# Kernel tuning notes

Hardware: AMD Instinct MI355X
Metric: run time of the kernel (lower is better)

The kernel has to match this reference:

```python
import jax, jax.numpy as jnp
import numpy as np

E = 1024  # hidden_size
H = 16    # num_heads
D = E // H  # head_dim
LN_EPS = 1e-5


def setup_inputs() -> dict:
    key = jax.random.key(0)
    ks = jax.random.split(key, 7)
    B, S = 4, 2048
    scale = 1.0 / np.sqrt(E)
    return {
        "txt_emb": jax.random.normal(ks[0], (B, S, E), dtype=jnp.float32),
        "in_proj_w": jax.random.normal(ks[1], (3 * E, E), dtype=jnp.float32) * scale,
        "in_proj_b": jnp.zeros((3 * E,), dtype=jnp.float32),
        "out_proj_w": jax.random.normal(ks[2], (E, E), dtype=jnp.float32) * scale,
        "out_proj_b": jnp.zeros((E,), dtype=jnp.float32),
        "ln_gamma": jnp.ones((E,), dtype=jnp.float32),
        "ln_beta": jnp.zeros((E,), dtype=jnp.float32),
    }


def _layer_norm(x, gamma, beta):
    mu = jnp.mean(x, axis=-1, keepdims=True)
    var = jnp.var(x, axis=-1, keepdims=True)
    return (x - mu) * jax.lax.rsqrt(var + LN_EPS) * gamma + beta


def reference(txt_emb, in_proj_w, in_proj_b, out_proj_w, out_proj_b, ln_gamma, ln_beta):
    B, S, _ = txt_emb.shape
    # joint QKV projection (torch nn.MultiheadAttention semantics: x @ W.T + b)
    qkv = jnp.einsum('bse,fe->bsf', txt_emb, in_proj_w) + in_proj_b  # [B,S,3E]
    q, k, v = jnp.split(qkv, 3, axis=-1)
    # [B,H,S,D]
    q = q.reshape(B, S, H, D).transpose(0, 2, 1, 3)
    k = k.reshape(B, S, H, D).transpose(0, 2, 1, 3)
    v = v.reshape(B, S, H, D).transpose(0, 2, 1, 3)
    scores = jnp.einsum('bhqd,bhkd->bhqk', q, k) / np.sqrt(D)  # [B,H,S,S]
    causal = jnp.tril(jnp.ones((S, S), dtype=bool))
    scores = jnp.where(causal, scores, jnp.float32(-jnp.inf))
    attn = jax.nn.softmax(scores, axis=-1)
    ctx = jnp.einsum('bhqk,bhkd->bhqd', attn, v)  # [B,H,S,D]
    ctx = ctx.transpose(0, 2, 1, 3).reshape(B, S, E)
    attn_out = jnp.einsum('bse,fe->bsf', ctx, out_proj_w) + out_proj_b
    return _layer_norm(txt_emb + attn_out, ln_gamma, ln_beta)
```

## Files before the change

### kernel.cpp

```cpp
#include <hip/hip_runtime.h>
#include <hip/hip_bf16.h>
#include <stdint.h>

#define B_   4
#define S_   2048
#define E_   1024
#define H_   16
#define D_   64
#define M_   (B_ * S_)
#define E3_  (3 * E_)

#define QSCALE 0.18033688011112042f

typedef __bf16 bf16_t;
typedef bf16_t bf16x8 __attribute__((ext_vector_type(8)));
typedef float  f32x4  __attribute__((ext_vector_type(4)));
typedef float  f32x16 __attribute__((ext_vector_type(16)));

__device__ __forceinline__ ushort f2bf(float f) {
  union { float f; uint32_t u; } v; v.f = f;
  uint32_t r = v.u + 0x7fffu + ((v.u >> 16) & 1u);
  return (ushort)(r >> 16);
}

__device__ __forceinline__ float bf2f(ushort u) {
  union { uint32_t u; float f; } v; v.u = ((uint32_t)u) << 16;
  return v.f;
}

__device__ __forceinline__ unsigned cvtpk(float lo, float hi_) {
  unsigned d;
  asm("v_cvt_pk_bf16_f32 %0, %1, %2" : "=v"(d) : "v"(lo), "v"(hi_));
  return d;
}

__device__ __forceinline__ void gload_lds16(const void* g, void* l) {
  __builtin_amdgcn_global_load_lds((const __attribute__((address_space(1))) void*)g,
                                   (__attribute__((address_space(3))) void*)l,
                                   16, 0, 0);
}

__global__ __launch_bounds__(256) void cvt_all(const float* __restrict__ x,
                                               const float* __restrict__ w_in,
                                               const float* __restrict__ w_out,
                                               ushort* __restrict__ xb,
                                               ushort* __restrict__ winb,
                                               ushort* __restrict__ woutb) {
  const int stride = gridDim.x * blockDim.x;
  for (int i = blockIdx.x * blockDim.x + threadIdx.x; i < 3145728; i += stride) {
    const float* src; ushort* dst; int j; float sc = 1.f;
    if (i < 2097152)      { src = x;     dst = xb;    j = i; }
    else if (i < 2883584) { src = w_in;  dst = winb;  j = i - 2097152; if (j < 262144) sc = QSCALE; }
    else                  { src = w_out; dst = woutb; j = i - 2883584; }
    float4 v = reinterpret_cast<const float4*>(src)[j];
    ushort4 o;
    o.x = f2bf(v.x * sc); o.y = f2bf(v.y * sc); o.z = f2bf(v.z * sc); o.w = f2bf(v.w * sc);
    reinterpret_cast<ushort4*>(dst)[j] = o;
  }
}

template <int MODE>
__global__ __launch_bounds__(256) void gemm_bt2(const ushort* __restrict__ A,
                                                const ushort* __restrict__ Bt,
                                                const float* __restrict__ bias,
                                                void* __restrict__ out0,
                                                ushort* __restrict__ vTout,
                                                int Ndim, int K) {
  __shared__ __align__(16) char lds[3][16384];

  const int tid  = threadIdx.x;
  const int lane = tid & 63, wid = tid >> 6;
  const int w = wid;
  const int wr = wid >> 1, wc = wid & 1;

  const int nx  = Ndim >> 7;
  const int nwg = gridDim.x;
  const int b0  = blockIdx.x;
  const int nb  = (b0 & 7) * (nwg >> 3) + (b0 >> 3);
  const int bm  = (nb / nx) * 128, bn = (nb % nx) * 128;

  const int srow  = tid >> 2;
  const int sslot = (tid & 3) ^ (srow & 3) ^ ((srow >> 2) & 3);
  const ushort* aS = A  + (size_t)(bm + srow) * K + sslot * 8;
  const ushort* bS = Bt + (size_t)(bn + srow) * K + sslot * 8;

#define STAGE_A(T, BUF)                                                          \
  do {                                                                           \
    gload_lds16(aS + (size_t)(T) * 32,              (void*)((BUF) + w * 1024));  \
    gload_lds16(aS + (size_t)(T) * 32 + 64 * K,     (void*)((BUF) + 4096 + w * 1024)); \
  } while (0)
#define STAGE_B(T, BUF)                                                          \
  do {                                                                           \
    gload_lds16(bS + (size_t)(T) * 32,              (void*)((BUF) + 8192 + w * 1024)); \
    gload_lds16(bS + (size_t)(T) * 32 + 64 * K,     (void*)((BUF) + 12288 + w * 1024)); \
  } while (0)

  const int lr15 = lane & 15;
  const int ksub = lane >> 4;
  const int slot = (ksub ^ (lr15 & 3) ^ ((lr15 >> 2) & 3)) * 16;
  const int arow_b = (wr * 64 + lr15) * 64;
  const int brow_b = 8192 + (wc * 64 + lr15) * 64;

#define LDA4(BUF)                                                                \
  do {                                                                           \
    _Pragma("unroll")                                                            \
    for (int rb = 0; rb < 4; ++rb)                                               \
      af[rb] = *(const bf16x8*)((BUF) + arow_b + rb * 1024 + slot);              \
  } while (0)
#define LDB2(BUF, CB)                                                            \
  do {                                                                           \
    _Pragma("unroll")                                                            \
    for (int n = 0; n < 2; ++n)                                                  \
      bfr[n] = *(const bf16x8*)((BUF) + brow_b + ((CB) + n) * 1024 + slot);      \
  } while (0)
#define MFMA8(CB)                                                                \
  do {                                                                           \
    __builtin_amdgcn_s_setprio(1);                                               \
    _Pragma("unroll")                                                            \
    for (int rb = 0; rb < 4; ++rb)                                               \
      _Pragma("unroll")                                                          \
      for (int n = 0; n < 2; ++n)                                                \
        acc[rb][(CB) + n] = __builtin_amdgcn_mfma_f32_16x16x32_bf16(             \
            af[rb], bfr[n], acc[rb][(CB) + n], 0, 0, 0);                         \
    __builtin_amdgcn_s_setprio(0);                                               \
  } while (0)

  f32x4 acc[4][4] = {};
  bf16x8 af[4], bfr[2];

  char* buf0 = &lds[0][0];
  char* buf1 = &lds[1][0];
  char* buf2 = &lds[2][0];

  const int nt = K >> 5;

  STAGE_A(0, buf0); STAGE_B(0, buf0);
  STAGE_A(1, buf1); STAGE_B(1, buf1);
  asm volatile("s_waitcnt vmcnt(4)" ::: "memory");
  __builtin_amdgcn_s_barrier();
  __builtin_amdgcn_sched_barrier(0);

  for (int t = 0; t < nt; ++t) {
    if (t < nt - 2) STAGE_A(t + 2, buf2);
    LDA4(buf0);
    LDB2(buf0, 0);
    __builtin_amdgcn_s_barrier();
    asm volatile("s_waitcnt lgkmcnt(0)" ::: "memory");
    __builtin_amdgcn_sched_barrier(0);
    MFMA8(0);
    __builtin_amdgcn_s_barrier();
    __builtin_amdgcn_sched_barrier(0);
    if (t < nt - 2) STAGE_B(t + 2, buf2);
    LDB2(buf0, 2);
    __builtin_amdgcn_s_barrier();
    asm volatile("s_waitcnt lgkmcnt(0)" ::: "memory");
    __builtin_amdgcn_sched_barrier(0);
    MFMA8(2);
    if (t < nt - 2) asm volatile("s_waitcnt vmcnt(4)" ::: "memory");
    else if (t == nt - 2) asm volatile("s_waitcnt vmcnt(0)" ::: "memory");
    __builtin_amdgcn_s_barrier();
    __builtin_amdgcn_sched_barrier(0);
    char* tmp = buf0; buf0 = buf1; buf1 = buf2; buf2 = tmp;
  }

#pragma unroll
  for (int rb = 0; rb < 4; ++rb) {
#pragma unroll
    for (int cb = 0; cb < 4; ++cb) {
      const int col = bn + wc * 64 + cb * 16 + lr15;
      float bv = bias[col];
      if (MODE == 1 && col < 1024) bv *= QSCALE;
      const int row0 = bm + wr * 64 + rb * 16 + ksub * 4;
      if (MODE == 0) {
#pragma unroll
        for (int r = 0; r < 4; ++r)
          ((ushort*)out0)[(size_t)(row0 + r) * Ndim + col] = f2bf(acc[rb][cb][r] + bv);
      } else {
        if (col < 2048) {
#pragma unroll
          for (int r = 0; r < 4; ++r)
            ((ushort*)out0)[(size_t)(row0 + r) * 2048 + col] = f2bf(acc[rb][cb][r] + bv);
        } else {
          ushort4 vv;
          vv.x = f2bf(acc[rb][cb][0] + bv);
          vv.y = f2bf(acc[rb][cb][1] + bv);
          vv.z = f2bf(acc[rb][cb][2] + bv);
          vv.w = f2bf(acc[rb][cb][3] + bv);
          const size_t vidx = ((size_t)((row0 >> 11) * 1024 + (col - 2048))) * 2048 + (row0 & 2047);
          *reinterpret_cast<ushort4*>(&vTout[vidx]) = vv;
        }
      }
    }
  }
#undef STAGE_A
#undef STAGE_B
#undef LDA4
#undef LDB2
#undef MFMA8
}

__global__ __launch_bounds__(512) void attn_causal(const ushort* __restrict__ qk,
                                                   const ushort* __restrict__ vT,
                                                   ushort* __restrict__ ctx) {
  __shared__ __align__(16) char lds[2][32768];

  const int tid = threadIdx.x;
  const int w = tid >> 6, lane = tid & 63;
  const int l31 = lane & 31, hi = lane >> 5;

  const int bid = blockIdx.x;
  const int bh = (bid & 7) * 8 + ((bid >> 3) & 7);
  const int g6 = bid >> 6;
  const int qb = (g6 < 4) ? (7 - g6) : (g6 - 4);
  const int b = bh >> 4, h = bh & 15;
  const int qw = qb * 256 + w * 32;
  const int q_g = qw + l31;
  const int my_tmax = (qw + 31) >> 6;
  const int U = 2 * qb + 2;

  const ushort* qrow = qk + (size_t)(b * S_ + q_g) * 2048 + h * 64;
  bf16x8 qf[4];
#pragma unroll
  for (int st = 0; st < 4; ++st)
    qf[st] = *reinterpret_cast<const bf16x8*>(qrow + st * 16 + hi * 8);

  const int srow = tid >> 3;
  const int swz  = ((tid & 7) * 16) ^ ((srow & 7) << 4);
  const char* kbase = (const char*)qk + ((size_t)(b * S_ + srow) * 2048 + 1024 + h * 64) * 2 + swz;
  const char* vbase = (const char*)vT + ((size_t)(bh * 64 + srow) * 2048) * 2 + swz;

  f32x16 Ot0 = {}, Ot1 = {};
  float m_r = -__builtin_inff(), l_r = 0.f;

  const int kswz = ((l31 & 7) << 4);

#define STAGE_PAIR(U2, BUFI)                                                            \
  do {                                                                                  \
    const size_t t0_ = (size_t)(U2) * 2;                                                \
    gload_lds16(kbase + t0_ * 262144,          &lds[BUFI][w * 1024]);                   \
    gload_lds16(kbase + (t0_ + 1) * 262144,    &lds[BUFI][8192 + w * 1024]);            \
    gload_lds16(vbase + t0_ * 128,             &lds[BUFI][16384 + w * 1024]);           \
    gload_lds16(vbase + t0_ * 128 + 128,       &lds[BUFI][24576 + w * 1024]);           \
  } while (0)

  STAGE_PAIR(0, 0);
  for (int u = 0; u < U; ++u) {
    const int bufi = u & 1;
    if (u < U - 1) {
      STAGE_PAIR(u + 1, bufi ^ 1);
      asm volatile("s_waitcnt vmcnt(4)" ::: "memory");
    } else {
      asm volatile("s_waitcnt vmcnt(0)" ::: "memory");
    }
    __builtin_amdgcn_s_barrier();
    __builtin_amdgcn_sched_barrier(0);

#pragma unroll
    for (int s = 0; s < 2; ++s) {
      const int t = 2 * u + s;
      if (t <= my_tmax) {
        const char* Kt = &lds[bufi][s * 8192];
        const char* Vp = &lds[bufi][16384 + s * 8192];

        f32x16 T0 = {}, T1 = {};
#pragma unroll
        for (int st = 0; st < 4; ++st) {
          const int cb = (st * 32 + hi * 16) ^ kswz;
          bf16x8 k0 = *(const bf16x8*)(Kt + l31 * 128 + cb);
          bf16x8 k1 = *(const bf16x8*)(Kt + (32 + l31) * 128 + cb);
          T0 = __builtin_amdgcn_mfma_f32_32x32x16_bf16(k0, qf[st], T0, 0, 0, 0);
          T1 = __builtin_amdgcn_mfma_f32_32x32x16_bf16(k1, qf[st], T1, 0, 0, 0);
        }

        float p[32];
        const bool needmask = (t * 64 + 63) > qw;
        const int kvb = t * 64 + 4 * hi;
#pragma unroll
        for (int g = 0; g < 4; ++g) {
#pragma unroll
          for (int j = 0; j < 4; ++j) {
            float v0 = T0[4 * g + j], v1 = T1[4 * g + j];
            if (needmask) {
              const int kv0 = kvb + 8 * g + j;
              v0 = (kv0      <= q_g) ? v0 : -__builtin_inff();
              v1 = (kv0 + 32 <= q_g) ? v1 : -__builtin_inff();
            }
            p[4 * g + j] = v0;
            p[16 + 4 * g + j] = v1;
          }
        }
        float pmax = p[0];
#pragma unroll
        for (int i = 1; i < 31; i += 2) pmax = fmaxf(fmaxf(pmax, p[i]), p[i + 1]);
        pmax = fmaxf(pmax, p[31]);
        pmax = fmaxf(pmax, __shfl_xor(pmax, 32));

        if (!__all(pmax - m_r <= 8.f)) {
          const float mn = fmaxf(m_r, pmax);
          const float sc = exp2f(m_r - mn);
          m_r = mn;
          l_r *= sc;
#pragma unroll
          for (int i = 0; i < 16; ++i) { Ot0[i] *= sc; Ot1[i] *= sc; }
        }
        float sum = 0.f;
#pragma unroll
        for (int i = 0; i < 32; ++i) { p[i] = exp2f(p[i] - m_r); sum += p[i]; }
        sum += __shfl_xor(sum, 32);
        l_r += sum;

#pragma unroll
        for (int ks = 0; ks < 4; ++ks) {
          const unsigned a = cvtpk(p[8 * ks + 0], p[8 * ks + 1]);
          const unsigned bq = cvtpk(p[8 * ks + 2], p[8 * ks + 3]);
          const unsigned c = cvtpk(p[8 * ks + 4], p[8 * ks + 5]);
          const unsigned d = cvtpk(p[8 * ks + 6], p[8 * ks + 7]);
          const unsigned x = hi ? a : c;
          const unsigned y = hi ? bq : d;
          const unsigned xp = (unsigned)__shfl_xor((int)x, 32);
          const unsigned yp = (unsigned)__shfl_xor((int)y, 32);
          union { unsigned u[4]; bf16x8 v; } pa;
          pa.u[0] = hi ? xp : a;
          pa.u[1] = hi ? yp : bq;
          pa.u[2] = hi ? c : xp;
          pa.u[3] = hi ? d : yp;
          const int cb = (ks * 32 + hi * 16) ^ kswz;
          bf16x8 v0 = *(const bf16x8*)(Vp + l31 * 128 + cb);
          bf16x8 v1 = *(const bf16x8*)(Vp + (32 + l31) * 128 + cb);
          Ot0 = __builtin_amdgcn_mfma_f32_32x32x16_bf16(v0, pa.v, Ot0, 0, 0, 0);
          Ot1 = __builtin_amdgcn_mfma_f32_32x32x16_bf16(v1, pa.v, Ot1, 0, 0, 0);
        }
      }
    }
    __builtin_amdgcn_s_barrier();
    __builtin_amdgcn_sched_barrier(0);
  }

  const float inv = 1.0f / l_r;
  ushort* crow = ctx + (size_t)(b * S_ + q_g) * 1024 + h * 64;
#pragma unroll
  for (int g = 0; g < 4; ++g) {
#pragma unroll
    for (int jp = 0; jp < 2; ++jp) {
      const int d0 = 2 * jp + 8 * g + 4 * hi;
      const int r = 4 * g + 2 * jp;
      *(unsigned*)(crow + d0)      = cvtpk(Ot0[r] * inv, Ot0[r + 1] * inv);
      *(unsigned*)(crow + 32 + d0) = cvtpk(Ot1[r] * inv, Ot1[r + 1] * inv);
    }
  }
#undef STAGE_PAIR
}

__global__ __launch_bounds__(256) void resid_ln(const float* __restrict__ x,
                                                const ushort* __restrict__ ao,
                                                const float* __restrict__ gamma,
                                                const float* __restrict__ beta,
                                                float* __restrict__ out) {
  const int row = blockIdx.x;
  const int tid = threadIdx.x;
  const size_t base = (size_t)row * E_;

  float4 xv = reinterpret_cast<const float4*>(x + base)[tid];
  ushort4 au = reinterpret_cast<const ushort4*>(ao + base)[tid];
  const float v0 = xv.x + bf2f(au.x), v1 = xv.y + bf2f(au.y);
  const float v2 = xv.z + bf2f(au.z), v3 = xv.w + bf2f(au.w);
  float s  = v0 + v1 + v2 + v3;
  float s2 = v0 * v0 + v1 * v1 + v2 * v2 + v3 * v3;
#pragma unroll
  for (int off = 32; off >= 1; off >>= 1) {
    s  += __shfl_xor(s, off);
    s2 += __shfl_xor(s2, off);
  }
  __shared__ float red[8];
  const int wid = tid >> 6, lane = tid & 63;
  if (lane == 0) { red[wid] = s; red[4 + wid] = s2; }
  __syncthreads();
  s  = red[0] + red[1] + red[2] + red[3];
  s2 = red[4] + red[5] + red[6] + red[7];
  const float mu  = s * (1.f / E_);
  const float var = s2 * (1.f / E_) - mu * mu;
  const float rsd = rsqrtf(var + 1e-5f);

  float4 gv = reinterpret_cast<const float4*>(gamma)[tid];
  float4 bv = reinterpret_cast<const float4*>(beta)[tid];
  float4 ov;
  ov.x = (v0 - mu) * rsd * gv.x + bv.x;
  ov.y = (v1 - mu) * rsd * gv.y + bv.y;
  ov.z = (v2 - mu) * rsd * gv.z + bv.z;
  ov.w = (v3 - mu) * rsd * gv.w + bv.w;
  reinterpret_cast<float4*>(out + base)[tid] = ov;
}

extern "C" void kernel_launch(void* const* d_in, const int* in_sizes, int n_in,
                              void* d_out, int out_size, void* d_ws, size_t ws_size,
                              hipStream_t stream) {
  (void)in_sizes; (void)n_in; (void)out_size; (void)ws_size;
  const float* x     = (const float*)d_in[0];
  const float* w_in  = (const float*)d_in[1];
  const float* b_in  = (const float*)d_in[2];
  const float* w_out = (const float*)d_in[3];
  const float* b_out = (const float*)d_in[4];
  const float* gamma = (const float*)d_in[5];
  const float* beta  = (const float*)d_in[6];
  float* out = (float*)d_out;

  char* ws = (char*)d_ws;
  ushort* xb    = (ushort*)(ws);
  ushort* winb  = (ushort*)(ws + 16777216);
  ushort* woutb = (ushort*)(ws + 23068672);
  ushort* qkb   = (ushort*)(ws + 25165824);
  ushort* vTb   = (ushort*)(ws + 58720256);
  ushort* ctxb  = (ushort*)(ws + 75497472);
  ushort* aob   = (ushort*)(ws + 92274688);

  cvt_all<<<dim3(2048), 256, 0, stream>>>(x, w_in, w_out, xb, winb, woutb);

  gemm_bt2<1><<<dim3(1536), 256, 0, stream>>>(xb, winb, b_in, qkb, vTb, E3_, E_);
  attn_causal<<<dim3(512), 512, 0, stream>>>(qkb, vTb, ctxb);
  gemm_bt2<0><<<dim3(512), 256, 0, stream>>>(ctxb, woutb, b_out, aob, nullptr, E_, E_);
  resid_ln<<<dim3(M_), 256, 0, stream>>>(x, aob, gamma, beta, out);
}
```

Measured before the change: 192.3 us.

## Split causal attention KV range across two blocks and merge partial outputs

Each attention block now handles only even or odd KV tiles for its query block, doubling the grid to 1024 blocks and halving LDS per block. Each half writes an unnormalized partial output and its (max, sum) statistics, and a new merge kernel rescales and combines the two halves into ctx. This aims to raise occupancy and parallelism for the long-tail causal blocks. It costs extra global traffic for the partial outputs, an additional kernel launch, and bf16 rounding of the unnormalized partials. The Op buffer overlaps the aob buffer, which is safe only because aob is written later.

```diff
diff --git a/kernel.cpp b/kernel.cpp
--- a/kernel.cpp
+++ b/kernel.cpp
@@ -201,22 +201,23 @@
 
 __global__ __launch_bounds__(512) void attn_causal(const ushort* __restrict__ qk,
                                                    const ushort* __restrict__ vT,
-                                                   ushort* __restrict__ ctx) {
-  __shared__ __align__(16) char lds[2][32768];
+                                                   ushort* __restrict__ Op,
+                                                   float2* __restrict__ ml) {
+  __shared__ __align__(16) char lds[2][16384];
 
   const int tid = threadIdx.x;
   const int w = tid >> 6, lane = tid & 63;
   const int l31 = lane & 31, hi = lane >> 5;
 
   const int bid = blockIdx.x;
-  const int bh = (bid & 7) * 8 + ((bid >> 3) & 7);
-  const int g6 = bid >> 6;
-  const int qb = (g6 < 4) ? (7 - g6) : (g6 - 4);
+  const int bh   = (bid & 7) * 8 + ((bid >> 3) & 7);
+  const int half = (bid >> 6) & 1;
+  const int qb   = 7 - (bid >> 7);
   const int b = bh >> 4, h = bh & 15;
   const int qw = qb * 256 + w * 32;
   const int q_g = qw + l31;
   const int my_tmax = (qw + 31) >> 6;
-  const int U = 2 * qb + 2;
+  const int niter = 2 * qb + 2;
 
   const ushort* qrow = qk + (size_t)(b * S_ + q_g) * 2048 + h * 64;
   bf16x8 qf[4];
@@ -234,121 +235,157 @@
 
   const int kswz = ((l31 & 7) << 4);
 
-#define STAGE_PAIR(U2, BUFI)                                                            \
-  do {                                                                                  \
-    const size_t t0_ = (size_t)(U2) * 2;                                                \
-    gload_lds16(kbase + t0_ * 262144,          &lds[BUFI][w * 1024]);                   \
-    gload_lds16(kbase + (t0_ + 1) * 262144,    &lds[BUFI][8192 + w * 1024]);            \
-    gload_lds16(vbase + t0_ * 128,             &lds[BUFI][16384 + w * 1024]);           \
-    gload_lds16(vbase + t0_ * 128 + 128,       &lds[BUFI][24576 + w * 1024]);           \
-  } while (0)
-
-  STAGE_PAIR(0, 0);
-  for (int u = 0; u < U; ++u) {
+#define STAGE(T, BUFI)                                                              \
+  do {                                                                              \
+    gload_lds16(kbase + (size_t)(T) * 262144, &lds[BUFI][w * 1024]);                \
+    gload_lds16(vbase + (size_t)(T) * 128,    &lds[BUFI][8192 + w * 1024]);         \
+  } while (0)
+
+  STAGE(half, 0);
+  for (int u = 0; u < niter; ++u) {
+    const int t = half + 2 * u;
     const int bufi = u & 1;
-    if (u < U - 1) {
-      STAGE_PAIR(u + 1, bufi ^ 1);
-      asm volatile("s_waitcnt vmcnt(4)" ::: "memory");
+    if (u < niter - 1) {
+      STAGE(t + 2, bufi ^ 1);
+      asm volatile("s_waitcnt vmcnt(2)" ::: "memory");
     } else {
       asm volatile("s_waitcnt vmcnt(0)" ::: "memory");
     }
     __builtin_amdgcn_s_barrier();
     __builtin_amdgcn_sched_barrier(0);
 
-#pragma unroll
-    for (int s = 0; s < 2; ++s) {
-      const int t = 2 * u + s;
-      if (t <= my_tmax) {
-        const char* Kt = &lds[bufi][s * 8192];
-        const char* Vp = &lds[bufi][16384 + s * 8192];
-
-        f32x16 T0 = {}, T1 = {};
-#pragma unroll
-        for (int st = 0; st < 4; ++st) {
-          const int cb = (st * 32 + hi * 16) ^ kswz;
-          bf16x8 k0 = *(const bf16x8*)(Kt + l31 * 128 + cb);
-          bf16x8 k1 = *(const bf16x8*)(Kt + (32 + l31) * 128 + cb);
-          T0 = __builtin_amdgcn_mfma_f32_32x32x16_bf16(k0, qf[st], T0, 0, 0, 0);
-          T1 = __builtin_amdgcn_mfma_f32_32x32x16_bf16(k1, qf[st], T1, 0, 0, 0);
-        }
-
-        float p[32];
-        const bool needmask = (t * 64 + 63) > qw;
-        const int kvb = t * 64 + 4 * hi;
-#pragma unroll
-        for (int g = 0; g < 4; ++g) {
-#pragma unroll
-          for (int j = 0; j < 4; ++j) {
-            float v0 = T0[4 * g + j], v1 = T1[4 * g + j];
-            if (needmask) {
-              const int kv0 = kvb + 8 * g + j;
-              v0 = (kv0      <= q_g) ? v0 : -__builtin_inff();
-              v1 = (kv0 + 32 <= q_g) ? v1 : -__builtin_inff();
-            }
-            p[4 * g + j] = v0;
-            p[16 + 4 * g + j] = v1;
+    if (t <= my_tmax) {
+      const char* Kt = &lds[bufi][0];
+      const char* Vp = &lds[bufi][8192];
+
+      f32x16 T0 = {}, T1 = {};
+#pragma unroll
+      for (int st = 0; st < 4; ++st) {
+        const int cb = (st * 32 + hi * 16) ^ kswz;
+        bf16x8 k0 = *(const bf16x8*)(Kt + l31 * 128 + cb);
+        bf16x8 k1 = *(const bf16x8*)(Kt + (32 + l31) * 128 + cb);
+        T0 = __builtin_amdgcn_mfma_f32_32x32x16_bf16(k0, qf[st], T0, 0, 0, 0);
+        T1 = __builtin_amdgcn_mfma_f32_32x32x16_bf16(k1, qf[st], T1, 0, 0, 0);
+      }
+
+      float p[32];
+      const bool needmask = (t * 64 + 63) > qw;
+      const int kvb = t * 64 + 4 * hi;
+#pragma unroll
+      for (int g = 0; g < 4; ++g) {
+#pragma unroll
+        for (int j = 0; j < 4; ++j) {
+          float v0 = T0[4 * g + j], v1 = T1[4 * g + j];
+          if (needmask) {
+            const int kv0 = kvb + 8 * g + j;
+            v0 = (kv0      <= q_g) ? v0 : -__builtin_inff();
+            v1 = (kv0 + 32 <= q_g) ? v1 : -__builtin_inff();
           }
-        }
-        float pmax = p[0];
-#pragma unroll
-        for (int i = 1; i < 31; i += 2) pmax = fmaxf(fmaxf(pmax, p[i]), p[i + 1]);
-        pmax = fmaxf(pmax, p[31]);
-        pmax = fmaxf(pmax, __shfl_xor(pmax, 32));
-
-        if (!__all(pmax - m_r <= 8.f)) {
-          const float mn = fmaxf(m_r, pmax);
-          const float sc = exp2f(m_r - mn);
-          m_r = mn;
-          l_r *= sc;
-#pragma unroll
-          for (int i = 0; i < 16; ++i) { Ot0[i] *= sc; Ot1[i] *= sc; }
-        }
-        float sum = 0.f;
-#pragma unroll
-        for (int i = 0; i < 32; ++i) { p[i] = exp2f(p[i] - m_r); sum += p[i]; }
-        sum += __shfl_xor(sum, 32);
-        l_r += sum;
-
-#pragma unroll
-        for (int ks = 0; ks < 4; ++ks) {
-          const unsigned a = cvtpk(p[8 * ks + 0], p[8 * ks + 1]);
-          const unsigned bq = cvtpk(p[8 * ks + 2], p[8 * ks + 3]);
-          const unsigned c = cvtpk(p[8 * ks + 4], p[8 * ks + 5]);
-          const unsigned d = cvtpk(p[8 * ks + 6], p[8 * ks + 7]);
-          const unsigned x = hi ? a : c;
-          const unsigned y = hi ? bq : d;
-          const unsigned xp = (unsigned)__shfl_xor((int)x, 32);
-          const unsigned yp = (unsigned)__shfl_xor((int)y, 32);
-          union { unsigned u[4]; bf16x8 v; } pa;
-          pa.u[0] = hi ? xp : a;
-          pa.u[1] = hi ? yp : bq;
-          pa.u[2] = hi ? c : xp;
-          pa.u[3] = hi ? d : yp;
-          const int cb = (ks * 32 + hi * 16) ^ kswz;
-          bf16x8 v0 = *(const bf16x8*)(Vp + l31 * 128 + cb);
-          bf16x8 v1 = *(const bf16x8*)(Vp + (32 + l31) * 128 + cb);
-          Ot0 = __builtin_amdgcn_mfma_f32_32x32x16_bf16(v0, pa.v, Ot0, 0, 0, 0);
-          Ot1 = __builtin_amdgcn_mfma_f32_32x32x16_bf16(v1, pa.v, Ot1, 0, 0, 0);
+          p[4 * g + j] = v0;
+          p[16 + 4 * g + j] = v1;
         }
       }
+      float pmax = p[0];
+#pragma unroll
+      for (int i = 1; i < 31; i += 2) pmax = fmaxf(fmaxf(pmax, p[i]), p[i + 1]);
+      pmax = fmaxf(pmax, p[31]);
+      pmax = fmaxf(pmax, __shfl_xor(pmax, 32));
+
+      if (!__all(pmax - m_r <= 8.f)) {
+        const float mn = fmaxf(m_r, pmax);
+        const float sc = exp2f(m_r - mn);
+        m_r = mn;
+        l_r *= sc;
+#pragma unroll
+        for (int i = 0; i < 16; ++i) { Ot0[i] *= sc; Ot1[i] *= sc; }
+      }
+      float sum = 0.f;
+#pragma unroll
+      for (int i = 0; i < 32; ++i) { p[i] = exp2f(p[i] - m_r); sum += p[i]; }
+      sum += __shfl_xor(sum, 32);
+      l_r += sum;
+
+#pragma unroll
+      for (int ks = 0; ks < 4; ++ks) {
+        const unsigned a = cvtpk(p[8 * ks + 0], p[8 * ks + 1]);
+        const unsigned bq = cvtpk(p[8 * ks + 2], p[8 * ks + 3]);
+        const unsigned c = cvtpk(p[8 * ks + 4], p[8 * ks + 5]);
+        const unsigned d = cvtpk(p[8 * ks + 6], p[8 * ks + 7]);
+        const unsigned x = hi ? a : c;
+        const unsigned y = hi ? bq : d;
+        const unsigned xp = (unsigned)__shfl_xor((int)x, 32);
+        const unsigned yp = (unsigned)__shfl_xor((int)y, 32);
+        union { unsigned u[4]; bf16x8 v; } pa;
+        pa.u[0] = hi ? xp : a;
+        pa.u[1] = hi ? yp : bq;
+        pa.u[2] = hi ? c : xp;
+        pa.u[3] = hi ? d : yp;
+        const int cb = (ks * 32 + hi * 16) ^ kswz;
+        bf16x8 v0 = *(const bf16x8*)(Vp + l31 * 128 + cb);
+        bf16x8 v1 = *(const bf16x8*)(Vp + (32 + l31) * 128 + cb);
+        Ot0 = __builtin_amdgcn_mfma_f32_32x32x16_bf16(v0, pa.v, Ot0, 0, 0, 0);
+        Ot1 = __builtin_amdgcn_mfma_f32_32x32x16_bf16(v1, pa.v, Ot1, 0, 0, 0);
+      }
     }
     __builtin_amdgcn_s_barrier();
     __builtin_amdgcn_sched_barrier(0);
   }
 
-  const float inv = 1.0f / l_r;
-  ushort* crow = ctx + (size_t)(b * S_ + q_g) * 1024 + h * 64;
+  ushort* orow = Op + ((size_t)(half * 64 + bh) * 2048 + q_g) * 64;
 #pragma unroll
   for (int g = 0; g < 4; ++g) {
 #pragma unroll
     for (int jp = 0; jp < 2; ++jp) {
       const int d0 = 2 * jp + 8 * g + 4 * hi;
       const int r = 4 * g + 2 * jp;
-      *(unsigned*)(crow + d0)      = cvtpk(Ot0[r] * inv, Ot0[r + 1] * inv);
-      *(unsigned*)(crow + 32 + d0) = cvtpk(Ot1[r] * inv, Ot1[r + 1] * inv);
+      *(unsigned*)(orow + d0)      = cvtpk(Ot0[r], Ot0[r + 1]);
+      *(unsigned*)(orow + 32 + d0) = cvtpk(Ot1[r], Ot1[r + 1]);
     }
   }
-#undef STAGE_PAIR
+  if (hi == 0) {
+    float2 v; v.x = m_r; v.y = l_r;
+    ml[(size_t)(half * 64 + bh) * 2048 + q_g] = v;
+  }
+#undef STAGE
+}
+
+__global__ __launch_bounds__(256) void attn_merge(const ushort* __restrict__ Op,
+                                                  const float2* __restrict__ ml,
+                                                  ushort* __restrict__ ctx) {
+  const int gid = blockIdx.x * 256 + threadIdx.x;
+  const int r = gid >> 3;
+  const int c8 = (gid & 7) * 8;
+  const int bh = r >> 11, q = r & 2047;
+  const float2 m0 = ml[r];
+  const float2 m1 = ml[131072 + r];
+  const float M = fmaxf(m0.x, m1.x);
+  const float a0 = exp2f(m0.x - M), a1 = exp2f(m1.x - M);
+  const float inv = 1.0f / (a0 * m0.y + a1 * m1.y);
+  const float s0 = a0 * inv, s1 = a1 * inv;
+
+  const size_t base = (size_t)r * 64 + c8;
+  ushort4 p0a = *(const ushort4*)(Op + base);
+  ushort4 p0b = *(const ushort4*)(Op + base + 4);
+  ushort4 p1a = *(const ushort4*)(Op + 8388608 + base);
+  ushort4 p1b = *(const ushort4*)(Op + 8388608 + base + 4);
+
+  float v[8];
+  v[0] = s0 * bf2f(p0a.x) + s1 * bf2f(p1a.x);
+  v[1] = s0 * bf2f(p0a.y) + s1 * bf2f(p1a.y);
+  v[2] = s0 * bf2f(p0a.z) + s1 * bf2f(p1a.z);
+  v[3] = s0 * bf2f(p0a.w) + s1 * bf2f(p1a.w);
+  v[4] = s0 * bf2f(p0b.x) + s1 * bf2f(p1b.x);
+  v[5] = s0 * bf2f(p0b.y) + s1 * bf2f(p1b.y);
+  v[6] = s0 * bf2f(p0b.z) + s1 * bf2f(p1b.z);
+  v[7] = s0 * bf2f(p0b.w) + s1 * bf2f(p1b.w);
+
+  uint4 o;
+  o.x = cvtpk(v[0], v[1]);
+  o.y = cvtpk(v[2], v[3]);
+  o.z = cvtpk(v[4], v[5]);
+  o.w = cvtpk(v[6], v[7]);
+  const size_t caddr = ((size_t)((bh >> 4) * 2048 + q)) * 1024 + (bh & 15) * 64 + c8;
+  *reinterpret_cast<uint4*>(ctx + caddr) = o;
 }
 
 __global__ __launch_bounds__(256) void resid_ln(const float* __restrict__ x,
@@ -411,12 +448,15 @@
   ushort* qkb   = (ushort*)(ws + 25165824);
   ushort* vTb   = (ushort*)(ws + 58720256);
   ushort* ctxb  = (ushort*)(ws + 75497472);
+  ushort* Opb   = (ushort*)(ws + 92274688);
+  float2* mlb   = (float2*)(ws + 125829120);
   ushort* aob   = (ushort*)(ws + 92274688);
 
   cvt_all<<<dim3(2048), 256, 0, stream>>>(x, w_in, w_out, xb, winb, woutb);
 
   gemm_bt2<1><<<dim3(1536), 256, 0, stream>>>(xb, winb, b_in, qkb, vTb, E3_, E_);
-  attn_causal<<<dim3(512), 512, 0, stream>>>(qkb, vTb, ctxb);
+  attn_causal<<<dim3(1024), 512, 0, stream>>>(qkb, vTb, Opb, mlb);
+  attn_merge<<<dim3(4096), 256, 0, stream>>>(Opb, mlb, ctxb);
   gemm_bt2<0><<<dim3(512), 256, 0, stream>>>(ctxb, woutb, b_out, aob, nullptr, E_, E_);
   resid_ln<<<dim3(M_), 256, 0, stream>>>(x, aob, gamma, beta, out);
 }
```

Measured after the change: 197.1 us. 2.5% more time.
